# Performance work log

Measured on AMD Instinct MI355X. Metric: run time of the kernel, lower is better.

Reference implementation:

```python
import jax, jax.numpy as jnp
import numpy as np

O, I, B, H, W = 128, 128, 32, 112, 112
STRIDE, PAD = 1, 1

def _synth_weight(core, periphery, threshold, scale):
    # core: (O,I,1,1); periphery: (8,); threshold: (O,); scale: (1,)
    c = core[:, :, 0, 0]                                   # (O,I) center tap
    # threshold-gated scale: soft gate on periphery contribution per (o,i)
    gate = jax.nn.sigmoid(scale[0] * (jnp.abs(c) - threshold[:, None]))  # (O,I)
    # 9 flattened taps: index 4 is center (weight 1), others use shared periphery
    p_full = jnp.concatenate([periphery[:4], jnp.ones((1,), c.dtype), periphery[4:]])  # (9,)
    is_center = (jnp.arange(9) == 4).astype(c.dtype)        # (9,)
    gate_k = is_center[None, None, :] + (1.0 - is_center)[None, None, :] * gate[:, :, None]
    w = c[:, :, None] * p_full[None, None, :] * gate_k      # (O,I,9)
    return w.reshape(c.shape[0], c.shape[1], 3, 3)          # (O,I,3,3)

def setup_inputs() -> dict:
    key = jax.random.key(0)
    kx, kc, kp = jax.random.split(key, 3)
    x = jax.random.normal(kx, (B, I, H, W), dtype=jnp.float32)
    # kaiming-uniform-ish core init
    bound = float(np.sqrt(6.0 / I))
    core = jax.random.uniform(kc, (O, I, 1, 1), minval=-bound, maxval=bound, dtype=jnp.float32)
    periphery = jax.random.uniform(kp, (8,), minval=-0.1, maxval=0.1, dtype=jnp.float32)
    threshold = jnp.full((O,), 0.1, dtype=jnp.float32)
    scale = jnp.array([10.0], dtype=jnp.float32)
    return {"x": x, "core": core, "periphery": periphery, "threshold": threshold, "scale": scale}

def reference(x, core, periphery, threshold, scale):
    w = _synth_weight(core, periphery, threshold, scale)    # (O,I,3,3)
    return jax.lax.conv_general_dilated(
        x, w,
        window_strides=(STRIDE, STRIDE),
        padding=[(PAD, PAD), (PAD, PAD)],
        dimension_numbers=("NCHW", "OIHW", "NCHW"),
    )
```

## Files before the change

kernel.cpp:

```cpp
#include <hip/hip_runtime.h>

typedef short short8 __attribute__((ext_vector_type(8)));
typedef float f32x4 __attribute__((ext_vector_type(4)));
typedef unsigned short ushort8_t __attribute__((ext_vector_type(8)));

#define O_CH 128
#define I_CH 128
#define HW 112
#define PLANE (HW * HW)
#define NCOL 114
#define BUFB (3 * NCOL * 64)

__device__ __forceinline__ unsigned short f2bf(float f) {
  union { float f; unsigned u; } v; v.f = f;
  unsigned r = v.u + 0x7FFFu + ((v.u >> 16) & 1u);
  return (unsigned short)(r >> 16);
}

__device__ __forceinline__ unsigned pktrunc(float lo, float hi) {
  union { float f; unsigned u; } a, b; a.f = lo; b.f = hi;
  return __builtin_amdgcn_perm(b.u, a.u, 0x07060302u);
}

__global__ void wsynth_kernel(const float* __restrict__ core,
                              const float* __restrict__ periph,
                              const float* __restrict__ thr,
                              const float* __restrict__ scale,
                              unsigned short* __restrict__ Wb) {
  int idx = blockIdx.x * blockDim.x + threadIdx.x;
  if (idx >= O_CH * I_CH) return;
  int o = idx >> 7;
  float c = core[idx];
  float s = scale[0];
  float g = 1.0f / (1.0f + __expf(-s * (fabsf(c) - thr[o])));
#pragma unroll
  for (int tap = 0; tap < 9; ++tap) {
    float p  = (tap == 4) ? 1.0f : periph[tap < 4 ? tap : tap - 1];
    float gg = (tap == 4) ? 1.0f : g;
    Wb[tap * (O_CH * I_CH) + idx] = f2bf(c * p * gg);
  }
}

__global__ __launch_bounds__(256, 3)
void conv_kernel(const float* __restrict__ X,
                 const unsigned short* __restrict__ Wb,
                 float* __restrict__ Out) {
  __shared__ unsigned short Xs[2 * 3 * NCOL * 32];
  char* lds = (char*)Xs;

  const int bid = blockIdx.x;
  const int L = (bid & 7) * 448 + (bid >> 3);
  const int b = L / HW;
  const int y = L - b * HW;

  const int t   = threadIdx.x;
  const int wv  = t >> 6;
  const int l   = t & 63;
  const int ln  = l & 15;
  const int lk4 = l >> 4;

  const int c    = t & 127;
  const int chb  = (t >> 7) * 16;
  const int icol = c - 1;
  const bool cok = (c < NCOL);
  const int wxor = (c & 3) ^ (((c >> 2) & 1) << 1);

  f32x4 acc[2][7];
#pragma unroll
  for (int mr = 0; mr < 2; ++mr)
#pragma unroll
    for (int nf = 0; nf < 7; ++nf)
      acc[mr][nf] = (f32x4)0.0f;

#define LOAD16(V, KCH, SUB)                                                     \
  {                                                                             \
    const int row_ = y + (SUB)-1;                                               \
    const bool ok_ = (row_ >= 0) && (row_ < HW) && (icol >= 0) && (icol < HW);  \
    const float* sp_ = X + ((size_t)(b * I_CH + (KCH) + chb) * HW + row_) * HW  \
                       + icol;                                                  \
    _Pragma("unroll") for (int j = 0; j < 16; ++j) V[j] = 0.0f;                 \
    if (ok_) {                                                                  \
      _Pragma("unroll") for (int j = 0; j < 16; ++j) V[j] = sp_[j * PLANE];     \
    }                                                                           \
  }

#define WRITE16(V, SUB, WB)                                                     \
  if (cok) {                                                                    \
    const int base_ = ((SUB)*NCOL + c) * 64;                                    \
    _Pragma("unroll") for (int q = 0; q < 2; ++q) {                             \
      union { ushort8_t s; unsigned u[4]; } pk_;                                \
      pk_.u[0] = pktrunc(V[q * 8 + 0], V[q * 8 + 1]);                           \
      pk_.u[1] = pktrunc(V[q * 8 + 2], V[q * 8 + 3]);                           \
      pk_.u[2] = pktrunc(V[q * 8 + 4], V[q * 8 + 5]);                           \
      pk_.u[3] = pktrunc(V[q * 8 + 6], V[q * 8 + 7]);                           \
      const int slot_ = ((chb >> 3) + q) ^ wxor;                                \
      *reinterpret_cast<ushort8_t*>((WB) + base_ + slot_ * 16) = pk_.s;         \
    }                                                                           \
  }

#define COMPUTE_SUB(SUB, RB, K)                                                 \
  _Pragma("unroll") for (int dx = 0; dx < 3; ++dx) {                            \
    const int tap_ = (SUB)*3 + dx;                                              \
    const unsigned short* wp_ = Wb + tap_ * (O_CH * I_CH)                       \
                              + (wv * 32 + ln) * I_CH + (K)*32 + lk4 * 8;       \
    short8 a0_ = *reinterpret_cast<const short8*>(wp_);                         \
    short8 a1_ = *reinterpret_cast<const short8*>(wp_ + 16 * I_CH);             \
    const int cc_ = dx + ln;                                                    \
    const int rslot_ = lk4 ^ (cc_ & 3) ^ (((cc_ >> 2) & 1) << 1);               \
    const char* bp_ = (RB) + ((SUB)*NCOL + cc_) * 64 + rslot_ * 16;             \
    _Pragma("unroll") for (int nf = 0; nf < 7; ++nf) {                          \
      short8 bb_ = *reinterpret_cast<const short8*>(bp_ + nf * 1024);           \
      acc[0][nf] = __builtin_amdgcn_mfma_f32_16x16x32_bf16(a0_, bb_, acc[0][nf], 0, 0, 0); \
      acc[1][nf] = __builtin_amdgcn_mfma_f32_16x16x32_bf16(a1_, bb_, acc[1][nf], 0, 0, 0); \
    }                                                                           \
  }

  {
    float P0[16], P1[16], P2[16];
    LOAD16(P0, 0, 0)
    LOAD16(P1, 0, 1)
    LOAD16(P2, 0, 2)
    WRITE16(P0, 0, lds)
    WRITE16(P1, 1, lds)
    WRITE16(P2, 2, lds)
  }
  __syncthreads();

#pragma unroll
  for (int k = 0; k < 4; ++k) {
    char* rbuf = lds + (k & 1) * BUFB;
    char* wbuf = lds + ((k & 1) ^ 1) * BUFB;
    float LA[16], LB[16];

    if (k < 3) LOAD16(LA, (k + 1) * 32, 0)
    COMPUTE_SUB(0, rbuf, k)

    if (k < 3) LOAD16(LB, (k + 1) * 32, 1)
    COMPUTE_SUB(1, rbuf, k)
    if (k < 3) WRITE16(LA, 0, wbuf)

    if (k < 3) LOAD16(LA, (k + 1) * 32, 2)
    COMPUTE_SUB(2, rbuf, k)
    if (k < 3) {
      WRITE16(LB, 1, wbuf)
      WRITE16(LA, 2, wbuf)
      __syncthreads();
    }
  }

  const int obase = wv * 32 + lk4 * 4;
  float* outp = Out + (size_t)b * O_CH * PLANE + (size_t)y * HW;
#pragma unroll
  for (int mr = 0; mr < 2; ++mr) {
#pragma unroll
    for (int j = 0; j < 4; ++j) {
      const int o = obase + mr * 16 + j;
      float* po = outp + (size_t)o * PLANE;
#pragma unroll
      for (int nf = 0; nf < 7; ++nf) {
        po[nf * 16 + ln] = acc[mr][nf][j];
      }
    }
  }
}

extern "C" void kernel_launch(void* const* d_in, const int* in_sizes, int n_in,
                              void* d_out, int out_size, void* d_ws, size_t ws_size,
                              hipStream_t stream) {
  const float* x      = (const float*)d_in[0];
  const float* core   = (const float*)d_in[1];
  const float* periph = (const float*)d_in[2];
  const float* thr    = (const float*)d_in[3];
  const float* scale  = (const float*)d_in[4];
  unsigned short* Wb  = (unsigned short*)d_ws;

  wsynth_kernel<<<(O_CH * I_CH + 255) / 256, 256, 0, stream>>>(core, periph, thr, scale, Wb);

  const int grid = 32 * HW;
  conv_kernel<<<grid, 256, 0, stream>>>(x, Wb, (float*)d_out);
}
```

Baseline: 207.0 us.

## Switch conv MFMA tiling to 32x32x16 with 2x2 wave grid over outputs and columns

Replaces the 16x16x32 MFMA tiling, where each wave owned 32 output channels across all 112 columns, with 32x32x16 MFMA tiles. The four waves now form a 2x2 grid, each covering 64 output channels by 64 columns. Weight fragments for all three dx taps are loaded into registers before each sub-row's compute. The LDS row buffer is padded to 130 columns with a new XOR swizzle, and the output store is rewritten for the 32x32 accumulator layout. This cuts LDS B-fragment reads per MFMA and improves operand reuse, but pads the work to 128 columns (about 14% wasted MFMA) and raises register pressure.

```diff
diff --git a/kernel.cpp b/kernel.cpp
--- a/kernel.cpp
+++ b/kernel.cpp
@@ -1,15 +1,16 @@
 #include <hip/hip_runtime.h>
 
 typedef short short8 __attribute__((ext_vector_type(8)));
-typedef float f32x4 __attribute__((ext_vector_type(4)));
+typedef float f32x16 __attribute__((ext_vector_type(16)));
 typedef unsigned short ushort8_t __attribute__((ext_vector_type(8)));
 
 #define O_CH 128
 #define I_CH 128
 #define HW 112
 #define PLANE (HW * HW)
-#define NCOL 114
-#define BUFB (3 * NCOL * 64)
+#define NCOLR 114
+#define NCOL2 130
+#define BUFB (3 * NCOL2 * 64)
 
 __device__ __forceinline__ unsigned short f2bf(float f) {
   union { float f; unsigned u; } v; v.f = f;
@@ -45,7 +46,7 @@
 void conv_kernel(const float* __restrict__ X,
                  const unsigned short* __restrict__ Wb,
                  float* __restrict__ Out) {
-  __shared__ unsigned short Xs[2 * 3 * NCOL * 32];
+  __shared__ unsigned short Xs[2 * 3 * NCOL2 * 32];
   char* lds = (char*)Xs;
 
   const int bid = blockIdx.x;
@@ -53,24 +54,26 @@
   const int b = L / HW;
   const int y = L - b * HW;
 
-  const int t   = threadIdx.x;
-  const int wv  = t >> 6;
-  const int l   = t & 63;
-  const int ln  = l & 15;
-  const int lk4 = l >> 4;
+  const int t    = threadIdx.x;
+  const int wv   = t >> 6;
+  const int l    = t & 63;
+  const int ln32 = l & 31;
+  const int hi2  = l >> 5;
+  const int mi   = wv >> 1;
+  const int ci   = wv & 1;
 
   const int c    = t & 127;
   const int chb  = (t >> 7) * 16;
   const int icol = c - 1;
-  const bool cok = (c < NCOL);
-  const int wxor = (c & 3) ^ (((c >> 2) & 1) << 1);
+  const bool cok = (c < NCOLR);
+  const int wxor = (c >> 1) & 3;
 
-  f32x4 acc[2][7];
+  f32x16 acc[2][2];
 #pragma unroll
-  for (int mr = 0; mr < 2; ++mr)
+  for (int mt = 0; mt < 2; ++mt)
 #pragma unroll
-    for (int nf = 0; nf < 7; ++nf)
-      acc[mr][nf] = (f32x4)0.0f;
+    for (int cf = 0; cf < 2; ++cf)
+      acc[mt][cf] = (f32x16)0.0f;
 
 #define LOAD16(V, KCH, SUB)                                                     \
   {                                                                             \
@@ -86,7 +89,7 @@
 
 #define WRITE16(V, SUB, WB)                                                     \
   if (cok) {                                                                    \
-    const int base_ = ((SUB)*NCOL + c) * 64;                                    \
+    const int base_ = ((SUB)*NCOL2 + c) * 64;                                   \
     _Pragma("unroll") for (int q = 0; q < 2; ++q) {                             \
       union { ushort8_t s; unsigned u[4]; } pk_;                                \
       pk_.u[0] = pktrunc(V[q * 8 + 0], V[q * 8 + 1]);                           \
@@ -98,20 +101,25 @@
     }                                                                           \
   }
 
-#define COMPUTE_SUB(SUB, RB, K)                                                 \
+#define APLOAD32(AF, SUB, K)                                                    \
+  _Pragma("unroll") for (int dx = 0; dx < 3; ++dx)                              \
+    _Pragma("unroll") for (int mt = 0; mt < 2; ++mt)                            \
+      _Pragma("unroll") for (int ks = 0; ks < 2; ++ks)                          \
+        AF[dx][mt][ks] = *reinterpret_cast<const short8*>(                      \
+            Wb + ((SUB)*3 + dx) * (O_CH * I_CH)                                 \
+               + (mi * 64 + mt * 32 + ln32) * I_CH + (K)*32 + ks * 16 + hi2 * 8);
+
+#define COMPUTE_SUB32(SUB, RB, AF)                                              \
   _Pragma("unroll") for (int dx = 0; dx < 3; ++dx) {                            \
-    const int tap_ = (SUB)*3 + dx;                                              \
-    const unsigned short* wp_ = Wb + tap_ * (O_CH * I_CH)                       \
-                              + (wv * 32 + ln) * I_CH + (K)*32 + lk4 * 8;       \
-    short8 a0_ = *reinterpret_cast<const short8*>(wp_);                         \
-    short8 a1_ = *reinterpret_cast<const short8*>(wp_ + 16 * I_CH);             \
-    const int cc_ = dx + ln;                                                    \
-    const int rslot_ = lk4 ^ (cc_ & 3) ^ (((cc_ >> 2) & 1) << 1);               \
-    const char* bp_ = (RB) + ((SUB)*NCOL + cc_) * 64 + rslot_ * 16;             \
-    _Pragma("unroll") for (int nf = 0; nf < 7; ++nf) {                          \
-      short8 bb_ = *reinterpret_cast<const short8*>(bp_ + nf * 1024);           \
-      acc[0][nf] = __builtin_amdgcn_mfma_f32_16x16x32_bf16(a0_, bb_, acc[0][nf], 0, 0, 0); \
-      acc[1][nf] = __builtin_amdgcn_mfma_f32_16x16x32_bf16(a1_, bb_, acc[1][nf], 0, 0, 0); \
+    _Pragma("unroll") for (int cf = 0; cf < 2; ++cf) {                          \
+      const int s_ = ci * 64 + cf * 32 + dx + ln32;                             \
+      _Pragma("unroll") for (int ks = 0; ks < 2; ++ks) {                        \
+        const int slot_ = (ks * 2 + hi2) ^ ((s_ >> 1) & 3);                     \
+        short8 bb_ = *reinterpret_cast<const short8*>(                          \
+            (RB) + ((SUB)*NCOL2 + s_) * 64 + slot_ * 16);                       \
+        acc[0][cf] = __builtin_amdgcn_mfma_f32_32x32x16_bf16(AF[dx][0][ks], bb_, acc[0][cf], 0, 0, 0); \
+        acc[1][cf] = __builtin_amdgcn_mfma_f32_32x32x16_bf16(AF[dx][1][ks], bb_, acc[1][cf], 0, 0, 0); \
+      }                                                                         \
     }                                                                           \
   }
 
@@ -131,16 +139,20 @@
     char* rbuf = lds + (k & 1) * BUFB;
     char* wbuf = lds + ((k & 1) ^ 1) * BUFB;
     float LA[16], LB[16];
+    short8 AF[3][2][2];
 
+    APLOAD32(AF, 0, k)
     if (k < 3) LOAD16(LA, (k + 1) * 32, 0)
-    COMPUTE_SUB(0, rbuf, k)
+    COMPUTE_SUB32(0, rbuf, AF)
 
+    APLOAD32(AF, 1, k)
     if (k < 3) LOAD16(LB, (k + 1) * 32, 1)
-    COMPUTE_SUB(1, rbuf, k)
+    COMPUTE_SUB32(1, rbuf, AF)
     if (k < 3) WRITE16(LA, 0, wbuf)
 
+    APLOAD32(AF, 2, k)
     if (k < 3) LOAD16(LA, (k + 1) * 32, 2)
-    COMPUTE_SUB(2, rbuf, k)
+    COMPUTE_SUB32(2, rbuf, AF)
     if (k < 3) {
       WRITE16(LB, 1, wbuf)
       WRITE16(LA, 2, wbuf)
@@ -148,17 +160,19 @@
     }
   }
 
-  const int obase = wv * 32 + lk4 * 4;
-  float* outp = Out + (size_t)b * O_CH * PLANE + (size_t)y * HW;
 #pragma unroll
-  for (int mr = 0; mr < 2; ++mr) {
+  for (int mt = 0; mt < 2; ++mt) {
 #pragma unroll
-    for (int j = 0; j < 4; ++j) {
-      const int o = obase + mr * 16 + j;
-      float* po = outp + (size_t)o * PLANE;
+    for (int cf = 0; cf < 2; ++cf) {
+      const int colb = ci * 64 + cf * 32 + ln32;
+      if (colb < HW) {
+        float* po = Out + (size_t)b * O_CH * PLANE + (size_t)y * HW + colb
+                  + (size_t)(mi * 64 + mt * 32) * PLANE;
 #pragma unroll
-      for (int nf = 0; nf < 7; ++nf) {
-        po[nf * 16 + ln] = acc[mr][nf][j];
+        for (int reg = 0; reg < 16; ++reg) {
+          const int row = (reg & 3) + 8 * (reg >> 2) + 4 * hi2;
+          po[(size_t)row * PLANE] = acc[mt][cf][reg];
+        }
       }
     }
   }
```

After: 337.2 us. 1.63x slower.

## Give each wave its own column strip and LDS region, dropping block barriers

Applied to the files above, without the earlier changes.

Work is now split so each wave computes all 128 output channels for a 28-column strip of the output row, rather than 32 channels across the full row. Each wave stages its own 34-column halo window into a private double-buffered LDS region, so the per-chunk __syncthreads calls are removed. Each wave now loads 8 weight fragments per tap and reuses each B fragment across them. The cost is more redundant weight-fragment global loads per wave, halo overlap between strips, and wasted MFMA lanes on the last 4 columns of the 32-wide tile. Skipping barriers relies on each wave writing and reading only its own LDS region, with no wave-level fence between the write and later reads.

```diff
diff --git a/kernel.cpp b/kernel.cpp
--- a/kernel.cpp
+++ b/kernel.cpp
@@ -8,8 +8,10 @@
 #define I_CH 128
 #define HW 112
 #define PLANE (HW * HW)
-#define NCOL 114
-#define BUFB (3 * NCOL * 64)
+#define NCOLW 34
+#define SUBB (NCOLW * 64)
+#define WBUF (3 * SUBB)
+#define WREG (2 * WBUF)
 
 __device__ __forceinline__ unsigned short f2bf(float f) {
   union { float f; unsigned u; } v; v.f = f;
@@ -42,10 +44,10 @@
 }
 
 __global__ __launch_bounds__(256, 3)
-void conv_kernel(const float* __restrict__ X,
-                 const unsigned short* __restrict__ Wb,
-                 float* __restrict__ Out) {
-  __shared__ unsigned short Xs[2 * 3 * NCOL * 32];
+void conv_wi(const float* __restrict__ X,
+             const unsigned short* __restrict__ Wb,
+             float* __restrict__ Out) {
+  __shared__ __align__(16) unsigned short Xs[4 * WREG / 2];
   char* lds = (char*)Xs;
 
   const int bid = blockIdx.x;
@@ -58,108 +60,119 @@
   const int l   = t & 63;
   const int ln  = l & 15;
   const int lk4 = l >> 4;
+  const int cb  = wv * 28;
 
-  const int c    = t & 127;
-  const int chb  = (t >> 7) * 16;
-  const int icol = c - 1;
-  const bool cok = (c < NCOL);
-  const int wxor = (c & 3) ^ (((c >> 2) & 1) << 1);
+  char* wbase = lds + wv * WREG;
 
-  f32x4 acc[2][7];
+  const int cu0  = l >> 2;
+  const int oct0 = l & 3;
+  const int u1   = l + 64;
+  const bool v1  = (u1 < 120);
+  const int cu1  = u1 >> 2;
+  const int oct1 = u1 & 3;
+
+  f32x4 acc[8][2];
 #pragma unroll
-  for (int mr = 0; mr < 2; ++mr)
+  for (int mt = 0; mt < 8; ++mt)
 #pragma unroll
-    for (int nf = 0; nf < 7; ++nf)
-      acc[mr][nf] = (f32x4)0.0f;
+    for (int nf = 0; nf < 2; ++nf)
+      acc[mt][nf] = (f32x4)0.0f;
 
-#define LOAD16(V, KCH, SUB)                                                     \
+#define SLOAD(V, K, SUB)                                                        \
   {                                                                             \
     const int row_ = y + (SUB)-1;                                               \
-    const bool ok_ = (row_ >= 0) && (row_ < HW) && (icol >= 0) && (icol < HW);  \
-    const float* sp_ = X + ((size_t)(b * I_CH + (KCH) + chb) * HW + row_) * HW  \
-                       + icol;                                                  \
-    _Pragma("unroll") for (int j = 0; j < 16; ++j) V[j] = 0.0f;                 \
-    if (ok_) {                                                                  \
-      _Pragma("unroll") for (int j = 0; j < 16; ++j) V[j] = sp_[j * PLANE];     \
+    const bool rok_ = (row_ >= 0) && (row_ < HW);                               \
+    {                                                                           \
+      const int ic_ = cb - 1 + cu0;                                             \
+      const bool ok_ = rok_ && (ic_ >= 0) && (ic_ < HW);                        \
+      const float* sp_ = X + ((size_t)(b * I_CH + (K)*32 + oct0 * 8) * HW       \
+                              + row_) * HW + ic_;                               \
+      _Pragma("unroll") for (int j = 0; j < 8; ++j)                             \
+        V[j] = ok_ ? sp_[j * PLANE] : 0.0f;                                     \
+    }                                                                           \
+    {                                                                           \
+      const int ic_ = cb - 1 + cu1;                                             \
+      const bool ok_ = v1 && rok_ && (ic_ >= 0) && (ic_ < HW);                  \
+      const float* sp_ = X + ((size_t)(b * I_CH + (K)*32 + oct1 * 8) * HW       \
+                              + row_) * HW + ic_;                               \
+      _Pragma("unroll") for (int j = 0; j < 8; ++j)                             \
+        V[8 + j] = ok_ ? sp_[j * PLANE] : 0.0f;                                 \
     }                                                                           \
   }
 
-#define WRITE16(V, SUB, WB)                                                     \
-  if (cok) {                                                                    \
-    const int base_ = ((SUB)*NCOL + c) * 64;                                    \
-    _Pragma("unroll") for (int q = 0; q < 2; ++q) {                             \
+#define SWRITE(V, SUB, BUFOFF)                                                  \
+  {                                                                             \
+    {                                                                           \
       union { ushort8_t s; unsigned u[4]; } pk_;                                \
-      pk_.u[0] = pktrunc(V[q * 8 + 0], V[q * 8 + 1]);                           \
-      pk_.u[1] = pktrunc(V[q * 8 + 2], V[q * 8 + 3]);                           \
-      pk_.u[2] = pktrunc(V[q * 8 + 4], V[q * 8 + 5]);                           \
-      pk_.u[3] = pktrunc(V[q * 8 + 6], V[q * 8 + 7]);                           \
-      const int slot_ = ((chb >> 3) + q) ^ wxor;                                \
-      *reinterpret_cast<ushort8_t*>((WB) + base_ + slot_ * 16) = pk_.s;         \
+      pk_.u[0] = pktrunc(V[0], V[1]);  pk_.u[1] = pktrunc(V[2], V[3]);          \
+      pk_.u[2] = pktrunc(V[4], V[5]);  pk_.u[3] = pktrunc(V[6], V[7]);          \
+      const int slot_ = oct0 ^ ((cu0 >> 1) & 3);                                \
+      *reinterpret_cast<ushort8_t*>(wbase + (BUFOFF) + (SUB)*SUBB + cu0 * 64    \
+                                    + slot_ * 16) = pk_.s;                      \
+    }                                                                           \
+    if (v1) {                                                                   \
+      union { ushort8_t s; unsigned u[4]; } pk_;                                \
+      pk_.u[0] = pktrunc(V[8], V[9]);   pk_.u[1] = pktrunc(V[10], V[11]);       \
+      pk_.u[2] = pktrunc(V[12], V[13]); pk_.u[3] = pktrunc(V[14], V[15]);       \
+      const int slot_ = oct1 ^ ((cu1 >> 1) & 3);                                \
+      *reinterpret_cast<ushort8_t*>(wbase + (BUFOFF) + (SUB)*SUBB + cu1 * 64    \
+                                    + slot_ * 16) = pk_.s;                      \
     }                                                                           \
   }
 
-#define COMPUTE_SUB(SUB, RB, K)                                                 \
+#define CSUB(SUB, BUFOFF, K)                                                    \
   _Pragma("unroll") for (int dx = 0; dx < 3; ++dx) {                            \
-    const int tap_ = (SUB)*3 + dx;                                              \
-    const unsigned short* wp_ = Wb + tap_ * (O_CH * I_CH)                       \
-                              + (wv * 32 + ln) * I_CH + (K)*32 + lk4 * 8;       \
-    short8 a0_ = *reinterpret_cast<const short8*>(wp_);                         \
-    short8 a1_ = *reinterpret_cast<const short8*>(wp_ + 16 * I_CH);             \
-    const int cc_ = dx + ln;                                                    \
-    const int rslot_ = lk4 ^ (cc_ & 3) ^ (((cc_ >> 2) & 1) << 1);               \
-    const char* bp_ = (RB) + ((SUB)*NCOL + cc_) * 64 + rslot_ * 16;             \
-    _Pragma("unroll") for (int nf = 0; nf < 7; ++nf) {                          \
-      short8 bb_ = *reinterpret_cast<const short8*>(bp_ + nf * 1024);           \
-      acc[0][nf] = __builtin_amdgcn_mfma_f32_16x16x32_bf16(a0_, bb_, acc[0][nf], 0, 0, 0); \
-      acc[1][nf] = __builtin_amdgcn_mfma_f32_16x16x32_bf16(a1_, bb_, acc[1][nf], 0, 0, 0); \
+    const unsigned short* wp_ = Wb + ((SUB)*3 + dx) * (O_CH * I_CH)             \
+                              + ln * I_CH + (K)*32 + lk4 * 8;                   \
+    short8 a_[8];                                                               \
+    _Pragma("unroll") for (int mt = 0; mt < 8; ++mt)                            \
+      a_[mt] = *reinterpret_cast<const short8*>(wp_ + mt * 16 * I_CH);          \
+    _Pragma("unroll") for (int nf = 0; nf < 2; ++nf) {                          \
+      const int col_ = dx + nf * 16 + ln;                                       \
+      const int slot_ = lk4 ^ ((col_ >> 1) & 3);                                \
+      short8 bb_ = *reinterpret_cast<const short8*>(                            \
+          wbase + (BUFOFF) + (SUB)*SUBB + col_ * 64 + slot_ * 16);              \
+      _Pragma("unroll") for (int mt = 0; mt < 8; ++mt)                          \
+        acc[mt][nf] = __builtin_amdgcn_mfma_f32_16x16x32_bf16(a_[mt], bb_,      \
+                                                              acc[mt][nf], 0, 0, 0); \
     }                                                                           \
   }
 
-  {
-    float P0[16], P1[16], P2[16];
-    LOAD16(P0, 0, 0)
-    LOAD16(P1, 0, 1)
-    LOAD16(P2, 0, 2)
-    WRITE16(P0, 0, lds)
-    WRITE16(P1, 1, lds)
-    WRITE16(P2, 2, lds)
-  }
-  __syncthreads();
+  float LA[16], LB[16];
+
+  SLOAD(LA, 0, 0) SWRITE(LA, 0, 0)
+  SLOAD(LA, 0, 1) SWRITE(LA, 1, 0)
+  SLOAD(LA, 0, 2) SWRITE(LA, 2, 0)
 
 #pragma unroll
   for (int k = 0; k < 4; ++k) {
-    char* rbuf = lds + (k & 1) * BUFB;
-    char* wbuf = lds + ((k & 1) ^ 1) * BUFB;
-    float LA[16], LB[16];
+    const int rb = (k & 1) * WBUF;
+    const int wb2 = ((k & 1) ^ 1) * WBUF;
 
-    if (k < 3) LOAD16(LA, (k + 1) * 32, 0)
-    COMPUTE_SUB(0, rbuf, k)
+    if (k < 3) SLOAD(LA, k + 1, 0)
+    CSUB(0, rb, k)
 
-    if (k < 3) LOAD16(LB, (k + 1) * 32, 1)
-    COMPUTE_SUB(1, rbuf, k)
-    if (k < 3) WRITE16(LA, 0, wbuf)
+    if (k < 3) SLOAD(LB, k + 1, 1)
+    CSUB(1, rb, k)
+    if (k < 3) SWRITE(LA, 0, wb2)
 
-    if (k < 3) LOAD16(LA, (k + 1) * 32, 2)
-    COMPUTE_SUB(2, rbuf, k)
+    if (k < 3) SLOAD(LA, k + 1, 2)
+    CSUB(2, rb, k)
     if (k < 3) {
-      WRITE16(LB, 1, wbuf)
-      WRITE16(LA, 2, wbuf)
-      __syncthreads();
+      SWRITE(LB, 1, wb2)
+      SWRITE(LA, 2, wb2)
     }
   }
 
-  const int obase = wv * 32 + lk4 * 4;
-  float* outp = Out + (size_t)b * O_CH * PLANE + (size_t)y * HW;
+  float* outp = Out + (size_t)b * O_CH * PLANE + (size_t)y * HW + cb;
 #pragma unroll
-  for (int mr = 0; mr < 2; ++mr) {
+  for (int mt = 0; mt < 8; ++mt) {
 #pragma unroll
     for (int j = 0; j < 4; ++j) {
-      const int o = obase + mr * 16 + j;
+      const int o = mt * 16 + lk4 * 4 + j;
       float* po = outp + (size_t)o * PLANE;
-#pragma unroll
-      for (int nf = 0; nf < 7; ++nf) {
-        po[nf * 16 + ln] = acc[mr][nf][j];
-      }
+      po[ln] = acc[mt][0][j];
+      if (ln < 12) po[16 + ln] = acc[mt][1][j];
     }
   }
 }
@@ -177,5 +190,5 @@
   wsynth_kernel<<<(O_CH * I_CH + 255) / 256, 256, 0, stream>>>(core, periph, thr, scale, Wb);
 
   const int grid = 32 * HW;
-  conv_kernel<<<grid, 256, 0, stream>>>(x, Wb, (float*)d_out);
+  conv_wi<<<grid, 256, 0, stream>>>(x, Wb, (float*)d_out);
 }
```

New measurement: 587.1 us. +183.6%, slower.
